# Optimization experiments

Hardware: AMD Instinct MI355X
Metric: run time of the kernel (lower is better)

The kernel has to match this reference:

```python
import jax, jax.numpy as jnp
import numpy as np

LOG2 = float(np.log(2.0))

def _ssp(x):
    # shifted softplus: ln(0.5*(exp(x)+1)) = softplus(x) - ln 2
    return jax.nn.softplus(x) - LOG2

def setup_inputs() -> dict:
    key = jax.random.key(0)
    ks = jax.random.split(key, 8)
    B, N, D = 32, 512, 1024
    H = D // 2
    s = lambda fan_in: 1.0 / np.sqrt(fan_in)
    return {
        "representation": jax.random.normal(ks[0], (B, N, D), jnp.float32),
        "R": jax.random.normal(ks[1], (B, N, 3), jnp.float32),
        "atom_mask": jnp.ones((B, N), jnp.float32),
        "W1": jax.random.normal(ks[2], (D, H), jnp.float32) * s(D),
        "b1": jnp.zeros((H,), jnp.float32),
        "W2": jax.random.normal(ks[3], (H, 1), jnp.float32) * s(H),
        "b2": jnp.zeros((1,), jnp.float32),
        "Wc1": jax.random.normal(ks[4], (D, H), jnp.float32) * s(D),
        "bc1": jnp.zeros((H,), jnp.float32),
        "Wc2": jax.random.normal(ks[5], (H, 1), jnp.float32) * s(H),
        "bc2": jnp.zeros((1,), jnp.float32),
    }

def reference(representation, R, atom_mask, W1, b1, W2, b2, Wc1, bc1, Wc2, bc2):
    B, N, _ = representation.shape
    # Atomwise pyramidal MLP: n_in -> n_in//2 (shifted softplus) -> 1
    yi = _ssp(jnp.einsum("bnd,dh->bnh", representation, W1) + b1)
    yi = jnp.einsum("bnh,ho->bno", yi, W2) + b2            # [B,N,1]
    # masked sum pool over atoms (mean=0, stddev=1 so standardize is identity)
    y = jnp.sum(yi * atom_mask[..., None], axis=1)          # [B,1]

    # pairwise distances with safe sqrt (diag is exactly zero)
    diff = R[:, None, :, :] - R[:, :, None, :]              # [B,N,N,3]
    d2 = jnp.sum(diff * diff, axis=-1)                      # [B,N,N]
    dist = jnp.where(d2 > 0, jnp.sqrt(jnp.where(d2 > 0, d2, 1.0)), 0.0)

    eye = jnp.eye(N, dtype=dist.dtype)
    tot_mask = atom_mask[:, None, :] * atom_mask[:, :, None] * (1.0 - eye)
    keep = (tot_mask != 0).astype(dist.dtype)               # [B,N,N]
    dist = dist * keep

    # charge net: Dense(n_in, n_in//2, ssp) -> Dense(n_in//2, 1)
    q = _ssp(jnp.einsum("bnd,dh->bnh", representation, Wc1) + bc1)
    q = jnp.einsum("bnh,ho->bno", q, Wc2) + bc2             # [B,N,1]

    inv2 = (1e-5 + dist) ** -2                              # [B,N,N]
    coulomb = q[:, :, 0][:, None, :] * inv2 * q             # [B,N,N] (q_j * inv * q_i)
    coulomb = coulomb * keep
    e = jnp.sum(coulomb, axis=(1, 2))                       # [B]

    return y + e[:, None]                                   # [B,1]
```

## Files before the change

kernel.cpp:

```cpp
#include <hip/hip_runtime.h>
#include <math.h>


typedef unsigned short u16;
typedef unsigned int u32;
typedef __bf16 bf16x8 __attribute__((ext_vector_type(8)));
typedef float f32x4 __attribute__((ext_vector_type(4)));

#define GK 1024
#define NT 16

#define GLOAD_LDS16(g, l) __builtin_amdgcn_global_load_lds( \
    (const __attribute__((address_space(1))) void*)(g),     \
    (__attribute__((address_space(3))) void*)(l), 16, 0, 0)

__device__ __forceinline__ u16 f2bf(float f) {
    u32 u = __float_as_uint(f);
    return (u16)((u + 0x7FFFu + ((u >> 16) & 1u)) >> 16);
}

__device__ __forceinline__ float ssp_f(float x) {
    return __logf(0.5f * (__expf(x) + 1.0f));
}

__device__ __forceinline__ float ssp_slow(float x) {
    return fmaxf(x, 0.0f) + log1pf(expf(-fabsf(x))) - 0.6931471805599453f;
}


__global__ __launch_bounds__(256) void prep(
    const float* __restrict__ rep, const float* __restrict__ W1,
    const float* __restrict__ Wc1, u16* __restrict__ Abf,
    u16* __restrict__ Btb, float* __restrict__ out)
{
    __shared__ float tile[32][33];
    const int blk = blockIdx.x;
    const int t = threadIdx.x;
    if (blk < 8192) {
        int i = (blk * 256 + t) * 8;
        float4 x = *(const float4*)(rep + i);
        float4 y = *(const float4*)(rep + i + 4);
        union { u16 h[8]; uint4 v; } o;
        o.h[0] = f2bf(x.x); o.h[1] = f2bf(x.y); o.h[2] = f2bf(x.z); o.h[3] = f2bf(x.w);
        o.h[4] = f2bf(y.x); o.h[5] = f2bf(y.y); o.h[6] = f2bf(y.z); o.h[7] = f2bf(y.w);
        *(uint4*)(Abf + i) = o.v;
        if (blk == 0 && t < 32) out[t] = 0.0f;
    } else {
        const int bb = blk - 8192;
        const int k0 = (bb & 31) * 32;
        const int n0 = (bb >> 5) * 32;
        const float* src = (n0 < 512) ? W1 : Wc1;
        const int ns0 = (n0 < 512) ? n0 : n0 - 512;
#pragma unroll
        for (int j = 0; j < 4; j++) {
            int idx = j * 256 + t;
            int kl = idx >> 5, nl = idx & 31;
            tile[kl][nl] = src[(size_t)(k0 + kl) * 512 + ns0 + nl];
        }
        __syncthreads();
#pragma unroll
        for (int j = 0; j < 4; j++) {
            int idx = j * 256 + t;
            int nl = idx >> 5, kl = idx & 31;
            Btb[(size_t)(n0 + nl) * 1024 + k0 + kl] = f2bf(tile[kl][nl]);
        }
    }
}


__global__ __launch_bounds__(512, 2) void gemm_mfma(
    const u16* __restrict__ A,
    const u16* __restrict__ Bt,
    const float* __restrict__ b1, const float* __restrict__ W2,
    const float* __restrict__ bc1, const float* __restrict__ Wc2,
    float* __restrict__ parts)
{
    __shared__ u16 smem[2][32768];

    const int blk = blockIdx.x;
    const int swz = ((blk & 7) << 5) | (blk >> 3);
    const int bm = swz >> 2;
    const int bn = swz & 3;
    const int tid = threadIdx.x;
    const int w = tid >> 6, lane = tid & 63;
    const int wm = w & 1, wn = w >> 1;
    const int lm = lane & 15, q = lane >> 4;

    f32x4 acc[8][4];
#pragma unroll
    for (int i = 0; i < 8; i++)
#pragma unroll
        for (int j = 0; j < 4; j++)
            acc[i][j] = (f32x4){0.0f, 0.0f, 0.0f, 0.0f};

    int goff[2][2];
#pragma unroll
    for (int h = 0; h < 2; h++)
#pragma unroll
        for (int p2 = 0; p2 < 2; p2++) {
            int ci = h * 1024 + (w * 2 + p2) * 64 + lane;
            int row = ci >> 3;
            int c = (ci & 7) ^ (row & 7);
            goff[h][p2] = row * GK + c * 8;
        }

    int arow[4], brow[2], aswz[2];
#pragma unroll
    for (int mi = 0; mi < 4; mi++) arow[mi] = (wm * 128 + mi * 16 + lm) * 64;
#pragma unroll
    for (int nj = 0; nj < 2; nj++) brow[nj] = (wn * 64 + nj * 16 + lm) * 64;
#pragma unroll
    for (int kk = 0; kk < 2; kk++) aswz[kk] = ((kk * 4 + q) ^ (lm & 7)) * 8;

    const u16* Ab = A + (size_t)bm * 256 * GK;
    const u16* Bb = Bt + (size_t)bn * 256 * GK;

#define STAGE_HT(G, RG, H, BUF) do {                                          \
    GLOAD_LDS16((G) + goff[H][0], &smem[BUF][(RG) + ((H) * 1024 + (w * 2 + 0) * 64) * 8]); \
    GLOAD_LDS16((G) + goff[H][1], &smem[BUF][(RG) + ((H) * 1024 + (w * 2 + 1) * 64) * 8]); \
} while (0)

#define READ_A(BUF, MH)                                                       \
    _Pragma("unroll") for (int mi = 0; mi < 4; mi++)                          \
    _Pragma("unroll") for (int kk = 0; kk < 2; kk++)                          \
        afr[mi][kk] = *(const bf16x8*)&smem[BUF][arow[mi] + (MH) * 4096 + aswz[kk]];

#define READ_B(BUF, NH, DST)                                                  \
    _Pragma("unroll") for (int nj = 0; nj < 2; nj++)                          \
    _Pragma("unroll") for (int kk = 0; kk < 2; kk++)                          \
        DST[nj][kk] = *(const bf16x8*)&smem[BUF][16384 + brow[nj] + (NH) * 2048 + aswz[kk]];

#define MFMA_QUAD(MH, NH, BF)                                                 \
    _Pragma("unroll") for (int kk = 0; kk < 2; kk++)                          \
    _Pragma("unroll") for (int mi = 0; mi < 4; mi++)                          \
    _Pragma("unroll") for (int nj = 0; nj < 2; nj++)                          \
        acc[(MH) * 4 + mi][(NH) * 2 + nj] = __builtin_amdgcn_mfma_f32_16x16x32_bf16( \
            afr[mi][kk], BF[nj][kk], acc[(MH) * 4 + mi][(NH) * 2 + nj], 0, 0, 0);

#pragma unroll
    for (int h = 0; h < 2; h++) {
        STAGE_HT(Ab, 0, h, 0);
        STAGE_HT(Bb, 16384, h, 0);
    }
    asm volatile("s_waitcnt vmcnt(0)" ::: "memory");
    __builtin_amdgcn_s_barrier();

    bf16x8 afr[4][2], b0f[2][2], b1f[2][2];
    READ_A(0, 0);
    READ_B(0, 0, b0f);

    for (int t = 0; t < NT; ++t) {
        const int cur = t & 1, nxt = cur ^ 1;
        const bool st = (t < NT - 1);
        const u16* gA = Ab + (t + 1) * 64;
        const u16* gB = Bb + (t + 1) * 64;

        if (st) {
            STAGE_HT(gA, 0, 0, nxt);
            STAGE_HT(gB, 16384, 0, nxt);
            STAGE_HT(gA, 0, 1, nxt);
            STAGE_HT(gB, 16384, 1, nxt);
        }

        READ_B(cur, 1, b1f);
        __builtin_amdgcn_s_setprio(1);
        MFMA_QUAD(0, 0, b0f);
        MFMA_QUAD(0, 1, b1f);
        __builtin_amdgcn_s_setprio(0);

        READ_A(cur, 1);
        __builtin_amdgcn_s_setprio(1);
        MFMA_QUAD(1, 1, b1f);
        MFMA_QUAD(1, 0, b0f);
        __builtin_amdgcn_s_setprio(0);

        asm volatile("s_waitcnt vmcnt(0)" ::: "memory");
        asm volatile("s_waitcnt lgkmcnt(0)" ::: "memory");
        __builtin_amdgcn_s_barrier();

        if (st) {
            READ_A(nxt, 0);
            READ_B(nxt, 0, b0f);
        }
    }

#undef STAGE_HT
#undef READ_A
#undef READ_B
#undef MFMA_QUAD

    __syncthreads();
    float* red = (float*)&smem[0][0];
    const bool is_q = (bn >= 2);
    const float* bb2 = is_q ? bc1 : b1;
    const float* vv = is_q ? Wc2 : W2;
    float bias[4], v[4];
#pragma unroll
    for (int nfr = 0; nfr < 4; nfr++) {
        int c = (bn & 1) * 256 + wn * 64 + nfr * 16 + lm;
        bias[nfr] = bb2[c];
        v[nfr] = vv[c];
    }
#pragma unroll
    for (int mfr = 0; mfr < 8; mfr++) {
#pragma unroll
        for (int r = 0; r < 4; r++) {
            float s = 0.0f;
#pragma unroll
            for (int nfr = 0; nfr < 4; nfr++)
                s += v[nfr] * ssp_f(acc[mfr][nfr][r] + bias[nfr]);
            s += __shfl_xor(s, 1);
            s += __shfl_xor(s, 2);
            s += __shfl_xor(s, 4);
            s += __shfl_xor(s, 8);
            if (lm == 0) red[wn * 256 + wm * 128 + mfr * 16 + q * 4 + r] = s;
        }
    }
    __syncthreads();
    if (tid < 256) {
        float val = red[0 * 256 + tid] + red[1 * 256 + tid] +
                    red[2 * 256 + tid] + red[3 * 256 + tid];
        parts[(size_t)bn * 16384 + bm * 256 + tid] = val;
    }
}


__global__ __launch_bounds__(256) void coulomb_k(
    const float* __restrict__ R, const float* __restrict__ mask,
    const float* __restrict__ parts, const float* __restrict__ b2p,
    const float* __restrict__ bc2p, float* __restrict__ out)
{
    const int N = 512;
    const int b = blockIdx.y;
    const int chunk = blockIdx.x;
    __shared__ float Rx[512], Ry[512], Rz[512], QM[512];
    __shared__ float rbuf[4];
    const int tid = threadIdx.x;
    const float bc2 = bc2p[0];
    const float b2 = b2p[0];

    for (int j = tid; j < N; j += 256) {
        int idx = b * N + j;
        float m = mask[idx];
        const float* rp = R + (size_t)idx * 3;
        Rx[j] = rp[0];
        Ry[j] = rp[1];
        Rz[j] = rp[2];
        float qv = parts[2 * 16384 + idx] + parts[3 * 16384 + idx] + bc2;
        QM[j] = qv * m;
    }
    __syncthreads();

    const int i = chunk * 64 + (tid & 63);
    const int js = (tid >> 6) * 128;
    const float xi = Rx[i], yi = Ry[i], zi = Rz[i], qmi = QM[i];
    float e = 0.0f;
    for (int j = js; j < js + 128; j++) {
        float dx = xi - Rx[j];
        float dy = yi - Ry[j];
        float dz = zi - Rz[j];
        float d2 = dx * dx + dy * dy + dz * dz;
        float t = 1e-5f + sqrtf(d2);
        float term = qmi * QM[j] / (t * t);
        e += (j == i) ? 0.0f : term;
    }
    if (tid < 64) {
        int ii = b * N + chunk * 64 + tid;
        float yv = parts[0 * 16384 + ii] + parts[1 * 16384 + ii] + b2;
        e += yv * mask[ii];
    }
    for (int off = 32; off > 0; off >>= 1) e += __shfl_down(e, off, 64);
    if ((tid & 63) == 0) rbuf[tid >> 6] = e;
    __syncthreads();
    if (tid == 0) atomicAdd(&out[b], rbuf[0] + rbuf[1] + rbuf[2] + rbuf[3]);
}


#define BM 128
#define BN 64
#define BK 16

__global__ __launch_bounds__(256) void mlp_gemm(
    const float* __restrict__ A, const float* __restrict__ W1,
    const float* __restrict__ Wc1, const float* __restrict__ b1,
    const float* __restrict__ bc1, const float* __restrict__ W2,
    const float* __restrict__ Wc2, float* __restrict__ yi_part,
    float* __restrict__ q_part)
{
    const int K = 1024;
    const int bm = blockIdx.x;
    const int bn = blockIdx.y;
    const bool is_q = (bn >= 8);
    const float* __restrict__ W = is_q ? Wc1 : W1;
    const int j0 = (bn & 7) * BN;

    __shared__ float As[BK][BM + 4];
    __shared__ float Bs[BK][BN + 4];
    __shared__ float red[BM];

    const int tid = threadIdx.x;
    const int tx = tid & 15;
    const int ty = tid >> 4;

    float acc[8][4];
#pragma unroll
    for (int r = 0; r < 8; r++)
#pragma unroll
        for (int c = 0; c < 4; c++) acc[r][c] = 0.0f;

    const int a_row = tid >> 2;
    const int a_k4 = (tid & 3) * 4;
    const float* Arow0 = A + (size_t)(bm * BM + a_row) * K;
    const float* Arow1 = Arow0 + (size_t)64 * K;
    const int w_k = tid >> 4;
    const int w_j = (tid & 15) * 4;

    for (int kt = 0; kt < K; kt += BK) {
        float4 av0 = *(const float4*)(Arow0 + kt + a_k4);
        float4 av1 = *(const float4*)(Arow1 + kt + a_k4);
        float4 wv = *(const float4*)(W + (size_t)(kt + w_k) * 512 + j0 + w_j);
        __syncthreads();
        As[a_k4 + 0][a_row] = av0.x;
        As[a_k4 + 1][a_row] = av0.y;
        As[a_k4 + 2][a_row] = av0.z;
        As[a_k4 + 3][a_row] = av0.w;
        As[a_k4 + 0][a_row + 64] = av1.x;
        As[a_k4 + 1][a_row + 64] = av1.y;
        As[a_k4 + 2][a_row + 64] = av1.z;
        As[a_k4 + 3][a_row + 64] = av1.w;
        *(float4*)&Bs[w_k][w_j] = wv;
        __syncthreads();
#pragma unroll
        for (int kk = 0; kk < BK; kk++) {
            float4 a0 = *(const float4*)&As[kk][ty * 8];
            float4 a1 = *(const float4*)&As[kk][ty * 8 + 4];
            float4 bv = *(const float4*)&Bs[kk][tx * 4];
            float ar[8] = {a0.x, a0.y, a0.z, a0.w, a1.x, a1.y, a1.z, a1.w};
            float bc[4] = {bv.x, bv.y, bv.z, bv.w};
#pragma unroll
            for (int r = 0; r < 8; r++)
#pragma unroll
                for (int c = 0; c < 4; c++)
                    acc[r][c] = fmaf(ar[r], bc[c], acc[r][c]);
        }
    }

    const float* bb = is_q ? bc1 : b1;
    const float* vv = is_q ? Wc2 : W2;
    float bias[4], v[4];
#pragma unroll
    for (int c = 0; c < 4; c++) {
        bias[c] = bb[j0 + tx * 4 + c];
        v[c] = vv[j0 + tx * 4 + c];
    }
    if (tid < BM) red[tid] = 0.0f;
    __syncthreads();
#pragma unroll
    for (int r = 0; r < 8; r++) {
        float s = 0.0f;
#pragma unroll
        for (int c = 0; c < 4; c++)
            s += v[c] * ssp_slow(acc[r][c] + bias[c]);
        atomicAdd(&red[ty * 8 + r], s);
    }
    __syncthreads();
    float* target = is_q ? q_part : yi_part;
    if (tid < BM) atomicAdd(&target[(size_t)bm * BM + tid], red[tid]);
}

__global__ __launch_bounds__(256) void coulomb_fb(
    const float* __restrict__ R, const float* __restrict__ mask,
    const float* __restrict__ yi_part, const float* __restrict__ q_part,
    const float* __restrict__ b2p, const float* __restrict__ bc2p,
    float* __restrict__ out)
{
    const int N = 512;
    const int b = blockIdx.y;
    const int chunk = blockIdx.x;
    __shared__ float Rx[512], Ry[512], Rz[512], QM[512];
    __shared__ float rbuf[4];
    const int tid = threadIdx.x;
    const float bc2 = bc2p[0];
    const float b2 = b2p[0];

    for (int j = tid; j < N; j += 256) {
        float m = mask[b * N + j];
        const float* rp = R + ((size_t)b * N + j) * 3;
        Rx[j] = rp[0];
        Ry[j] = rp[1];
        Rz[j] = rp[2];
        QM[j] = (q_part[b * N + j] + bc2) * m;
    }
    __syncthreads();

    const int i = chunk * 64 + (tid & 63);
    const int js = (tid >> 6) * 128;
    const float xi = Rx[i], yi = Ry[i], zi = Rz[i], qmi = QM[i];
    float e = 0.0f;
    for (int j = js; j < js + 128; j++) {
        float dx = xi - Rx[j];
        float dy = yi - Ry[j];
        float dz = zi - Rz[j];
        float d2 = dx * dx + dy * dy + dz * dz;
        float t = 1e-5f + sqrtf(d2);
        float term = qmi * QM[j] / (t * t);
        e += (j == i) ? 0.0f : term;
    }
    if (tid < 64) {
        int ii = chunk * 64 + tid;
        e += (yi_part[b * N + ii] + b2) * mask[b * N + ii];
    }
    for (int off = 32; off > 0; off >>= 1) e += __shfl_down(e, off, 64);
    if ((tid & 63) == 0) rbuf[tid >> 6] = e;
    __syncthreads();
    if (tid == 0) atomicAdd(&out[b], rbuf[0] + rbuf[1] + rbuf[2] + rbuf[3]);
}


extern "C" void kernel_launch(void* const* d_in, const int* in_sizes, int n_in,
                              void* d_out, int out_size, void* d_ws, size_t ws_size,
                              hipStream_t stream) {
    const float* rep  = (const float*)d_in[0];
    const float* R    = (const float*)d_in[1];
    const float* mask = (const float*)d_in[2];
    const float* W1   = (const float*)d_in[3];
    const float* b1   = (const float*)d_in[4];
    const float* W2   = (const float*)d_in[5];
    const float* b2   = (const float*)d_in[6];
    const float* Wc1  = (const float*)d_in[7];
    const float* bc1  = (const float*)d_in[8];
    const float* Wc2  = (const float*)d_in[9];
    const float* bc2  = (const float*)d_in[10];
    float* out = (float*)d_out;

    const size_t szA = 16384ull * 1024 * 2;
    const size_t szB = 1024ull * 1024 * 2;
    const size_t szP = 8ull * 16384 * 4;
    const size_t need = szA + szB + szP;

    if (ws_size >= need) {
        u16* Abf = (u16*)d_ws;
        u16* Btb = (u16*)((char*)d_ws + szA);
        float* parts = (float*)((char*)d_ws + szA + szB);

        prep<<<8192 + 1024, 256, 0, stream>>>(rep, W1, Wc1, Abf, Btb, out);
        gemm_mfma<<<256, 512, 0, stream>>>(Abf, Btb, b1, W2, bc1, Wc2, parts);
        coulomb_k<<<dim3(8, 32), 256, 0, stream>>>(R, mask, parts, b2, bc2, out);
    } else {
        float* yi_part = (float*)d_ws;
        float* q_part = yi_part + 16384;
        hipMemsetAsync(d_ws, 0, 2 * 16384 * sizeof(float), stream);
        hipMemsetAsync(d_out, 0, 32 * sizeof(float), stream);
        mlp_gemm<<<dim3(128, 16), 256, 0, stream>>>(rep, W1, Wc1, b1, bc1, W2, Wc2,
                                                    yi_part, q_part);
        coulomb_fb<<<dim3(8, 32), 256, 0, stream>>>(R, mask, yi_part, q_part, b2, bc2, out);
    }
}
```

Baseline: 166.1 us.

## Interleave per-half global-to-LDS staging with MFMA phases using partial vmcnt waits

Restructures the GEMM main loop so that each half-tile of A and B is staged into the next LDS buffer between MFMA quads, rather than all four stages being issued at the top. Partial s_waitcnt vmcnt counts replace full drains, and barriers are placed mid-iteration so loads can stay in flight across compute phases. The last iteration now issues redundant wrap-around loads instead of branching, and a final vmcnt(0) drains them. The intent is to hide more global load latency behind MFMA work, at the cost of extra barriers per iteration and wasted final-iteration traffic. It also relies on the vmcnt counts matching the number of loads each STAGE_HT issues.

Measured after the change: 168.7 us. About the same (+1.5%).

```diff
diff --git a/kernel.cpp b/kernel.cpp
--- a/kernel.cpp
+++ b/kernel.cpp
@@ -137,52 +137,50 @@
         acc[(MH) * 4 + mi][(NH) * 2 + nj] = __builtin_amdgcn_mfma_f32_16x16x32_bf16( \
             afr[mi][kk], BF[nj][kk], acc[(MH) * 4 + mi][(NH) * 2 + nj], 0, 0, 0);
 
-#pragma unroll
-    for (int h = 0; h < 2; h++) {
-        STAGE_HT(Ab, 0, h, 0);
-        STAGE_HT(Bb, 16384, h, 0);
-    }
-    asm volatile("s_waitcnt vmcnt(0)" ::: "memory");
+    STAGE_HT(Ab, 0, 0, 0);
+    STAGE_HT(Bb, 16384, 0, 0);
+    STAGE_HT(Bb, 16384, 1, 0);
+    STAGE_HT(Ab, 0, 1, 0);
+    asm volatile("s_waitcnt vmcnt(4)" ::: "memory");
     __builtin_amdgcn_s_barrier();
 
     bf16x8 afr[4][2], b0f[2][2], b1f[2][2];
-    READ_A(0, 0);
-    READ_B(0, 0, b0f);
 
     for (int t = 0; t < NT; ++t) {
         const int cur = t & 1, nxt = cur ^ 1;
-        const bool st = (t < NT - 1);
-        const u16* gA = Ab + (t + 1) * 64;
-        const u16* gB = Bb + (t + 1) * 64;
-
-        if (st) {
-            STAGE_HT(gA, 0, 0, nxt);
-            STAGE_HT(gB, 16384, 0, nxt);
-            STAGE_HT(gA, 0, 1, nxt);
-            STAGE_HT(gB, 16384, 1, nxt);
-        }
+        const u16* gA = Ab + ((t + 1) & (NT - 1)) * 64;
+        const u16* gB = Bb + ((t + 1) & (NT - 1)) * 64;
+
+        STAGE_HT(gA, 0, 0, nxt);
+        READ_A(cur, 0);
+        READ_B(cur, 0, b0f);
+        __builtin_amdgcn_s_setprio(1);
+        MFMA_QUAD(0, 0, b0f);
+        __builtin_amdgcn_s_setprio(0);
+        STAGE_HT(gB, 16384, 0, nxt);
+        asm volatile("s_waitcnt vmcnt(6)" ::: "memory");
+        __builtin_amdgcn_s_barrier();
 
         READ_B(cur, 1, b1f);
         __builtin_amdgcn_s_setprio(1);
-        MFMA_QUAD(0, 0, b0f);
         MFMA_QUAD(0, 1, b1f);
         __builtin_amdgcn_s_setprio(0);
+        STAGE_HT(gB, 16384, 1, nxt);
+        asm volatile("s_waitcnt vmcnt(6)" ::: "memory");
+        __builtin_amdgcn_s_barrier();
 
         READ_A(cur, 1);
         __builtin_amdgcn_s_setprio(1);
         MFMA_QUAD(1, 1, b1f);
+        __builtin_amdgcn_s_setprio(0);
+        STAGE_HT(gA, 0, 1, nxt);
+        __builtin_amdgcn_s_setprio(1);
         MFMA_QUAD(1, 0, b0f);
         __builtin_amdgcn_s_setprio(0);
-
-        asm volatile("s_waitcnt vmcnt(0)" ::: "memory");
-        asm volatile("s_waitcnt lgkmcnt(0)" ::: "memory");
+        asm volatile("s_waitcnt vmcnt(4) lgkmcnt(0)" ::: "memory");
         __builtin_amdgcn_s_barrier();
-
-        if (st) {
-            READ_A(nxt, 0);
-            READ_B(nxt, 0, b0f);
-        }
-    }
+    }
+    asm volatile("s_waitcnt vmcnt(0)" ::: "memory");
 
 #undef STAGE_HT
 #undef READ_A
```
